# Kernel tuning notes

Hardware: AMD Instinct MI355X
Metric: run time of the kernel (lower is better)

The kernel has to match this reference:

```python
import jax, jax.numpy as jnp
import numpy as np

BRANCH = 4
DEPTH = 8  # complete 4-ary tree, levels 0..8 (leaves are level 0)
X_SIZE = 512
H_SIZE = 512


def _build_tree():
    N = sum(BRANCH ** d for d in range(DEPTH + 1))  # 87381
    depth = np.zeros(N, dtype=np.int32)
    start = 1
    for d in range(1, DEPTH + 1):
        c = BRANCH ** d
        depth[start:start + c] = d
        start += c
    node_level = (DEPTH - depth).astype(np.int32)  # topological height, leaves=0
    src = np.arange(1, N, dtype=np.int32)          # child
    dst = (src - 1) // BRANCH                      # parent
    return N, src, dst.astype(np.int32), node_level


def setup_inputs() -> dict:
    key = jax.random.key(0)
    k = jax.random.split(key, 6)
    N, src, dst, node_level = _build_tree()
    sx = 1.0 / np.sqrt(X_SIZE)
    sh = 1.0 / np.sqrt(H_SIZE)
    return {
        "x": jax.random.normal(k[0], (N, X_SIZE), jnp.float32),
        "W_w": jax.random.normal(k[1], (3 * H_SIZE, X_SIZE), jnp.float32) * sx,
        "b_w": jax.random.normal(k[2], (3 * H_SIZE,), jnp.float32) * sx,
        "U_r": jax.random.normal(k[3], (H_SIZE, H_SIZE), jnp.float32) * sh,
        "U_hc": jax.random.normal(k[4], (H_SIZE, H_SIZE), jnp.float32) * sh,
        "U_z": jax.random.normal(k[5], (H_SIZE, H_SIZE), jnp.float32) * sh,
        "edge_src": jnp.asarray(src),
        "edge_dst": jnp.asarray(dst),
        "node_level": jnp.asarray(node_level),
        "num_levels": DEPTH + 1,
    }


def reference(x, W_w, b_w, U_r, U_hc, U_z, edge_src, edge_dst, node_level, num_levels):
    hs = U_r.shape[0]
    n = x.shape[0]
    wx = x @ W_w.T + b_w                      # (n, 3h)
    wrx = wx[:, :hs]
    whx = wx[:, hs:2 * hs]
    wzx = wx[:, 2 * hs:]
    edge_level = node_level[edge_dst]         # level of parent receiving the message

    # Leaves: mailbox is a single zero 'z' slot -> z = sigmoid(w_z_x), h_pre = 0
    h_leaf = (1.0 - jax.nn.sigmoid(wzx)) * jnp.tanh(whx)
    h = jnp.where((node_level == 0)[:, None], h_leaf, 0.0)

    for l in range(1, num_levels):
        emask = (edge_level == l).astype(x.dtype)[:, None]   # (E,1)
        hsrc = h[edge_src] * emask                            # masked child states (E,h)
        h_sum = jax.ops.segment_sum(hsrc, edge_dst, num_segments=n)  # sum of children
        r = jax.nn.sigmoid(wrx + h_sum @ U_r.T)
        h_cand = jnp.tanh(whx + (r * h_sum) @ U_hc.T)
        z_e = hsrc @ U_z.T                                    # raw U_z(h_child), (E,h)
        # reduce: h_pre = sum_children z_raw * h_child (no sigmoid, faithful to source)
        h_pre = jax.ops.segment_sum(z_e * hsrc, edge_dst, num_segments=n)
        # update: z = sigmoid(z_raw + w_z_x), summed over children
        z_sig_sum = jax.ops.segment_sum(
            jax.nn.sigmoid(z_e + wzx[edge_dst]) * emask, edge_dst, num_segments=n)
        h_new = h_pre + (1.0 - z_sig_sum) * h_cand
        h = jnp.where((node_level == l)[:, None], h_new, h)
    return h
```

## Files before the change

### kernel.cpp

```cpp
#include <hip/hip_runtime.h>


#define NNODES 87381
#define NINT   21845
#define NLEAF  65536

typedef __attribute__((ext_vector_type(8))) __bf16 bf16x8;
typedef __attribute__((ext_vector_type(4))) float f32x4;

__device__ __forceinline__ float sigmoidf_(float x) { return 1.0f / (1.0f + __expf(-x)); }
__device__ __forceinline__ float tanhf_(float x) { return 2.0f / (1.0f + __expf(-2.0f * x)) - 1.0f; }

__device__ __forceinline__ unsigned short bf_rne(float f) {
  unsigned int u = __float_as_uint(f);
  unsigned int r = u + 0x7FFFu + ((u >> 16) & 1u);
  return (unsigned short)(r >> 16);
}
__device__ __forceinline__ void split2(float f, unsigned short& h, unsigned short& l) {
  h = bf_rne(f);
  l = bf_rne(f - __uint_as_float((unsigned int)h << 16));
}
__device__ __forceinline__ float bf2f(unsigned short h) {
  return __uint_as_float((unsigned int)h << 16);
}

__global__ __launch_bounds__(256) void split_k(const float* __restrict__ s,
                                               unsigned short* __restrict__ hi,
                                               unsigned short* __restrict__ lo, int n4) {
  int i = blockIdx.x * 256 + threadIdx.x;
  if (i >= n4) return;
  float4 v = *(const float4*)(s + (size_t)i * 4);
  ushort4 h, l;
  split2(v.x, h.x, l.x); split2(v.y, h.y, l.y);
  split2(v.z, h.z, l.z); split2(v.w, h.w, l.w);
  *(ushort4*)(hi + (size_t)i * 4) = h;
  *(ushort4*)(lo + (size_t)i * 4) = l;
}

template <bool CLAMP>
__device__ __forceinline__ void stage_tile(const unsigned short* __restrict__ g,
                                           int rows_left, unsigned short* l0,
                                           int lane) {
#pragma unroll
  for (int c = 0; c < 8; ++c) {
    const int lr = c * 16 + (lane >> 2);
    const int gr = CLAMP ? (lr < rows_left ? lr : rows_left - 1) : lr;
    const int sg = (lane & 3) ^ ((lr >> 1) & 3);
    __builtin_amdgcn_global_load_lds(
        (const __attribute__((address_space(1))) void*)(g + (size_t)gr * 512 + sg * 8),
        (__attribute__((address_space(3))) void*)(l0 + c * 512), 16, 0, 0);
  }
}

template <int EPI>
__global__ __launch_bounds__(256) void mgemm(const unsigned short* __restrict__ Ah,
                                             const unsigned short* __restrict__ Al,
                                             const unsigned short* __restrict__ Bh,
                                             const unsigned short* __restrict__ Bl,
                                             float* __restrict__ C, int ldc, int M,
                                             const float* __restrict__ wx, int g0,
                                             const float* __restrict__ bias,
                                             const unsigned short* __restrict__ FH,
                                             const unsigned short* __restrict__ FL,
                                             unsigned short* __restrict__ Oh,
                                             unsigned short* __restrict__ Ol) {
  __shared__ unsigned short As_h[2][128][32];
  __shared__ unsigned short As_l[2][128][32];
  __shared__ unsigned short Bs_h[2][128][32];
  __shared__ unsigned short Bs_l[2][128][32];
  const int t = threadIdx.x;
  const int lane = t & 63, wave = t >> 6;
  const int wm = wave & 1, wn = wave >> 1;
  const int m0 = blockIdx.x * 128, n0 = blockIdx.y * 128;

  f32x4 acc[4][4];
#pragma unroll
  for (int i = 0; i < 4; ++i)
#pragma unroll
    for (int j = 0; j < 4; ++j) acc[i][j] = (f32x4){0.f, 0.f, 0.f, 0.f};

  const int fr = lane & 15, fg = lane >> 4;

  auto stage = [&](int buf, int k0) {
    if (wave == 0)      stage_tile<true >(Ah + (size_t)m0 * 512 + k0, M - m0, &As_h[buf][0][0], lane);
    else if (wave == 1) stage_tile<true >(Al + (size_t)m0 * 512 + k0, M - m0, &As_l[buf][0][0], lane);
    else if (wave == 2) stage_tile<false>(Bh + (size_t)n0 * 512 + k0, 0, &Bs_h[buf][0][0], lane);
    else                stage_tile<false>(Bl + (size_t)n0 * 512 + k0, 0, &Bs_l[buf][0][0], lane);
  };

  auto comp = [&](int buf) {
    bf16x8 ah[4], al[4], bh[4], bl[4];
#pragma unroll
    for (int mt = 0; mt < 4; ++mt) {
      const int row = wm * 64 + mt * 16 + fr;
      const int gp = (fg ^ ((row >> 1) & 3)) * 8;
      ah[mt] = *(const bf16x8*)&As_h[buf][row][gp];
      al[mt] = *(const bf16x8*)&As_l[buf][row][gp];
    }
#pragma unroll
    for (int nt = 0; nt < 4; ++nt) {
      const int row = wn * 64 + nt * 16 + fr;
      const int gp = (fg ^ ((row >> 1) & 3)) * 8;
      bh[nt] = *(const bf16x8*)&Bs_h[buf][row][gp];
      bl[nt] = *(const bf16x8*)&Bs_l[buf][row][gp];
    }
#pragma unroll
    for (int mt = 0; mt < 4; ++mt)
#pragma unroll
      for (int nt = 0; nt < 4; ++nt) {
        acc[mt][nt] = __builtin_amdgcn_mfma_f32_16x16x32_bf16(ah[mt], bh[nt], acc[mt][nt], 0, 0, 0);
        acc[mt][nt] = __builtin_amdgcn_mfma_f32_16x16x32_bf16(ah[mt], bl[nt], acc[mt][nt], 0, 0, 0);
        acc[mt][nt] = __builtin_amdgcn_mfma_f32_16x16x32_bf16(al[mt], bh[nt], acc[mt][nt], 0, 0, 0);
      }
  };

  stage(0, 0);
  __syncthreads();
  for (int kk = 0; kk < 16; kk += 2) {
    stage(1, (kk + 1) * 32);
    comp(0);
    __syncthreads();
    if (kk < 14) stage(0, (kk + 2) * 32);
    comp(1);
    __syncthreads();
  }

  const int ecol = lane & 15;
  const int erow = (lane >> 4) * 4;

  if (EPI == 4) {
#pragma unroll
    for (int mt = 0; mt < 4; ++mt) {
#pragma unroll
      for (int nt = 0; nt < 4; ++nt) {
        const int col = n0 + wn * 64 + nt * 16 + ecol;
        const int row0 = m0 + wm * 64 + mt * 16 + erow;
        if (row0 >= M) continue;
        const int p = row0 >> 2;
        const float wz = wx[(size_t)(g0 + p) * 1536 + 1024 + col];
        float hpre = 0.f, zs = 0.f;
#pragma unroll
        for (int r = 0; r < 4; ++r) {
          const float zev = acc[mt][nt][r];
          const float hch = bias[(size_t)(row0 + r) * 512 + col];
          hpre = fmaf(zev, hch, hpre);
          zs += sigmoidf_(zev + wz);
        }
        float* po = C + (size_t)p * 512 + col;
        const float hc = *po;
        const float res = hpre + (1.f - zs) * hc;
        *po = res;
        unsigned short oh, ol;
        split2(res, oh, ol);
        Oh[(size_t)p * 512 + col] = oh;
        Ol[(size_t)p * 512 + col] = ol;
      }
    }
    return;
  }

#pragma unroll
  for (int mt = 0; mt < 4; ++mt) {
#pragma unroll
    for (int nt = 0; nt < 4; ++nt) {
      const int col = n0 + wn * 64 + nt * 16 + ecol;
#pragma unroll
      for (int r = 0; r < 4; ++r) {
        const int row = m0 + wm * 64 + mt * 16 + erow + r;
        if (row >= M) continue;
        const float v = acc[mt][nt][r];
        if (EPI == 1) {
          const size_t ix = (size_t)row * 512 + col;
          const float hs = bf2f(FH[ix]) + bf2f(FL[ix]);
          const float rg = sigmoidf_(wx[(size_t)(g0 + row) * 1536 + col] + v);
          unsigned short oh, ol;
          split2(rg * hs, oh, ol);
          Oh[ix] = oh;
          Ol[ix] = ol;
        } else if (EPI == 2) {
          C[(size_t)row * ldc + col] = tanhf_(wx[(size_t)(g0 + row) * 1536 + 512 + col] + v);
        } else {
          C[(size_t)row * ldc + col] = v + bias[col];
        }
      }
    }
  }
}

__global__ __launch_bounds__(256) void mleaf(const unsigned short* __restrict__ xh,
                                             const unsigned short* __restrict__ xl,
                                             const unsigned short* __restrict__ Wh,
                                             const unsigned short* __restrict__ Wl,
                                             const float* __restrict__ bw,
                                             float* __restrict__ out,
                                             unsigned short* __restrict__ hcH,
                                             unsigned short* __restrict__ hcL) {
  __shared__ unsigned short As_h[2][128][32];
  __shared__ unsigned short As_l[2][128][32];
  __shared__ unsigned short Bs_h[2][128][32];
  __shared__ unsigned short Bs_l[2][128][32];
  const int t = threadIdx.x;
  const int lane = t & 63, wave = t >> 6;
  const int wm = wave & 1, wn = wave >> 1;
  const int m0 = blockIdx.x * 128, n0 = blockIdx.y * 64;

  f32x4 acch[4][2], accz[4][2];
#pragma unroll
  for (int i = 0; i < 4; ++i)
#pragma unroll
    for (int j = 0; j < 2; ++j) {
      acch[i][j] = (f32x4){0.f, 0.f, 0.f, 0.f};
      accz[i][j] = (f32x4){0.f, 0.f, 0.f, 0.f};
    }

  const int fr = lane & 15, fg = lane >> 4;

  auto stage = [&](int buf, int k0) {
    if (wave == 0) {
      stage_tile<false>(xh + (size_t)m0 * 512 + k0, 0, &As_h[buf][0][0], lane);
    } else if (wave == 1) {
      stage_tile<false>(xl + (size_t)m0 * 512 + k0, 0, &As_l[buf][0][0], lane);
    } else {
      const unsigned short* Ws = (wave == 2) ? Wh : Wl;
      unsigned short* dst = (wave == 2) ? &Bs_h[buf][0][0] : &Bs_l[buf][0][0];
#pragma unroll
      for (int c = 0; c < 8; ++c) {
        const int lr = c * 16 + (lane >> 2);
        const int grow = (lr < 64) ? (512 + n0 + lr) : (1024 + n0 + (lr - 64));
        const int sg = (lane & 3) ^ ((lr >> 1) & 3);
        __builtin_amdgcn_global_load_lds(
            (const __attribute__((address_space(1))) void*)(Ws + (size_t)grow * 512 + k0 + sg * 8),
            (__attribute__((address_space(3))) void*)(dst + c * 512), 16, 0, 0);
      }
    }
  };

  auto comp = [&](int buf) {
    bf16x8 ah[4], al[4], bhh[2], bhl[2], bzh[2], bzl[2];
#pragma unroll
    for (int mt = 0; mt < 4; ++mt) {
      const int row = wm * 64 + mt * 16 + fr;
      const int gp = (fg ^ ((row >> 1) & 3)) * 8;
      ah[mt] = *(const bf16x8*)&As_h[buf][row][gp];
      al[mt] = *(const bf16x8*)&As_l[buf][row][gp];
    }
#pragma unroll
    for (int nt = 0; nt < 2; ++nt) {
      const int rh_ = wn * 32 + nt * 16 + fr;
      const int rz_ = 64 + rh_;
      const int gph = (fg ^ ((rh_ >> 1) & 3)) * 8;
      const int gpz = (fg ^ ((rz_ >> 1) & 3)) * 8;
      bhh[nt] = *(const bf16x8*)&Bs_h[buf][rh_][gph];
      bhl[nt] = *(const bf16x8*)&Bs_l[buf][rh_][gph];
      bzh[nt] = *(const bf16x8*)&Bs_h[buf][rz_][gpz];
      bzl[nt] = *(const bf16x8*)&Bs_l[buf][rz_][gpz];
    }
#pragma unroll
    for (int mt = 0; mt < 4; ++mt)
#pragma unroll
      for (int nt = 0; nt < 2; ++nt) {
        acch[mt][nt] = __builtin_amdgcn_mfma_f32_16x16x32_bf16(ah[mt], bhh[nt], acch[mt][nt], 0, 0, 0);
        acch[mt][nt] = __builtin_amdgcn_mfma_f32_16x16x32_bf16(ah[mt], bhl[nt], acch[mt][nt], 0, 0, 0);
        acch[mt][nt] = __builtin_amdgcn_mfma_f32_16x16x32_bf16(al[mt], bhh[nt], acch[mt][nt], 0, 0, 0);
        accz[mt][nt] = __builtin_amdgcn_mfma_f32_16x16x32_bf16(ah[mt], bzh[nt], accz[mt][nt], 0, 0, 0);
        accz[mt][nt] = __builtin_amdgcn_mfma_f32_16x16x32_bf16(ah[mt], bzl[nt], accz[mt][nt], 0, 0, 0);
        accz[mt][nt] = __builtin_amdgcn_mfma_f32_16x16x32_bf16(al[mt], bzh[nt], accz[mt][nt], 0, 0, 0);
      }
  };

  stage(0, 0);
  __syncthreads();
  for (int kk = 0; kk < 16; kk += 2) {
    stage(1, (kk + 1) * 32);
    comp(0);
    __syncthreads();
    if (kk < 14) stage(0, (kk + 2) * 32);
    comp(1);
    __syncthreads();
  }

  const int ecol = lane & 15;
  const int erow = (lane >> 4) * 4;
#pragma unroll
  for (int mt = 0; mt < 4; ++mt) {
#pragma unroll
    for (int nt = 0; nt < 2; ++nt) {
      const int col = n0 + wn * 32 + nt * 16 + ecol;
      const float bh_ = bw[512 + col];
      const float bz_ = bw[1024 + col];
#pragma unroll
      for (int r = 0; r < 4; ++r) {
        const int row = m0 + wm * 64 + mt * 16 + erow + r;
        const float vh = acch[mt][nt][r] + bh_;
        const float vz = accz[mt][nt][r] + bz_;
        const float hval = (1.f - sigmoidf_(vz)) * tanhf_(vh);
        out[(size_t)(NINT + row) * 512 + col] = hval;
        unsigned short oh, ol;
        split2(hval, oh, ol);
        const size_t ix = (size_t)row * 512 + col;
        hcH[ix] = oh;
        hcL[ix] = ol;
      }
    }
  }
}

__global__ __launch_bounds__(256) void child_sum_k(const float* __restrict__ out,
                                                   int cbase, int nl,
                                                   unsigned short* __restrict__ hH,
                                                   unsigned short* __restrict__ hL) {
  const int idx = blockIdx.x * 256 + threadIdx.x;
  if (idx >= nl * 128) return;
  const int i = idx >> 7;
  const int jq = (idx & 127) << 2;
  const float* b = out + (size_t)(cbase + 4 * i) * 512 + jq;
  const float4 a = *(const float4*)(b);
  const float4 c = *(const float4*)(b + 512);
  const float4 d = *(const float4*)(b + 1024);
  const float4 e = *(const float4*)(b + 1536);
  float4 s;
  s.x = a.x + c.x + d.x + e.x;
  s.y = a.y + c.y + d.y + e.y;
  s.z = a.z + c.z + d.z + e.z;
  s.w = a.w + c.w + d.w + e.w;
  ushort4 sh, sl;
  split2(s.x, sh.x, sl.x); split2(s.y, sh.y, sl.y);
  split2(s.z, sh.z, sl.z); split2(s.w, sh.w, sl.w);
  *(ushort4*)(hH + (size_t)i * 512 + jq) = sh;
  *(ushort4*)(hL + (size_t)i * 512 + jq) = sl;
}

extern "C" void kernel_launch(void* const* d_in, const int* in_sizes, int n_in,
                              void* d_out, int out_size, void* d_ws, size_t ws_size,
                              hipStream_t stream) {
  const float* x   = (const float*)d_in[0];
  const float* Ww  = (const float*)d_in[1];
  const float* bw  = (const float*)d_in[2];
  const float* Ur  = (const float*)d_in[3];
  const float* Uhc = (const float*)d_in[4];
  const float* Uz  = (const float*)d_in[5];
  float* out = (float*)d_out;

  char* p = (char*)d_ws;
  unsigned short* x_hi = (unsigned short*)p;
  unsigned short* x_lo = x_hi + (size_t)NNODES * 512;
  unsigned short* rhH = (unsigned short*)p;
  unsigned short* rhL = rhH + (size_t)16384 * 512;
  p += (size_t)NNODES * 512 * 4;
  float* wx_int = (float*)p;                 p += (size_t)NINT * 1536 * 4;
  unsigned short* hsH = (unsigned short*)p;  p += (size_t)16384 * 512 * 2;
  unsigned short* hsL = (unsigned short*)p;  p += (size_t)16384 * 512 * 2;
  unsigned short* hcH = (unsigned short*)p;  p += (size_t)65536 * 512 * 2;
  unsigned short* hcL = (unsigned short*)p;  p += (size_t)65536 * 512 * 2;
  unsigned short* hc2H = (unsigned short*)p; p += (size_t)16384 * 512 * 2;
  unsigned short* hc2L = (unsigned short*)p; p += (size_t)16384 * 512 * 2;
  unsigned short* W_hi = (unsigned short*)p;   p += (size_t)1536 * 512 * 2;
  unsigned short* W_lo = (unsigned short*)p;   p += (size_t)1536 * 512 * 2;
  unsigned short* Ur_hi = (unsigned short*)p;  p += (size_t)512 * 512 * 2;
  unsigned short* Ur_lo = (unsigned short*)p;  p += (size_t)512 * 512 * 2;
  unsigned short* Uhc_hi = (unsigned short*)p; p += (size_t)512 * 512 * 2;
  unsigned short* Uhc_lo = (unsigned short*)p; p += (size_t)512 * 512 * 2;
  unsigned short* Uz_hi = (unsigned short*)p;  p += (size_t)512 * 512 * 2;
  unsigned short* Uz_lo = (unsigned short*)p;  p += (size_t)512 * 512 * 2;

  split_k<<<(1536 * 512 / 4 + 255) / 256, 256, 0, stream>>>(Ww, W_hi, W_lo, 1536 * 512 / 4);
  split_k<<<(512 * 512 / 4 + 255) / 256, 256, 0, stream>>>(Ur, Ur_hi, Ur_lo, 512 * 512 / 4);
  split_k<<<(512 * 512 / 4 + 255) / 256, 256, 0, stream>>>(Uhc, Uhc_hi, Uhc_lo, 512 * 512 / 4);
  split_k<<<(512 * 512 / 4 + 255) / 256, 256, 0, stream>>>(Uz, Uz_hi, Uz_lo, 512 * 512 / 4);
  split_k<<<((int)((size_t)NNODES * 512 / 4) + 255) / 256, 256, 0, stream>>>(
      x, x_hi, x_lo, (int)((size_t)NNODES * 512 / 4));

  mgemm<3><<<dim3((NINT + 127) / 128, 12), 256, 0, stream>>>(
      x_hi, x_lo, W_hi, W_lo, wx_int, 1536, NINT, nullptr, 0, bw,
      nullptr, nullptr, nullptr, nullptr);

  mleaf<<<dim3(NLEAF / 128, 8), 256, 0, stream>>>(
      x_hi + (size_t)NINT * 512, x_lo + (size_t)NINT * 512, W_hi, W_lo, bw, out, hcH, hcL);

  static const int S[10] = {0, 1, 5, 21, 85, 341, 1365, 5461, 21845, 87381};
  unsigned short *rdH = hcH, *rdL = hcL, *wrH = hc2H, *wrL = hc2L;
  for (int l = 1; l <= 8; ++l) {
    const int d = 8 - l;
    const int pbase = S[d];
    const int nl = S[d + 1] - S[d];
    const int cbase = S[d + 1];
    const int el = 4 * nl;

    child_sum_k<<<(nl * 128 + 255) / 256, 256, 0, stream>>>(out, cbase, nl, hsH, hsL);

    dim3 gr((nl + 127) / 128, 4);
    mgemm<1><<<gr, 256, 0, stream>>>(hsH, hsL, Ur_hi, Ur_lo, nullptr, 512, nl,
                                     wx_int, pbase, nullptr, hsH, hsL, rhH, rhL);
    mgemm<2><<<gr, 256, 0, stream>>>(rhH, rhL, Uhc_hi, Uhc_lo,
                                     out + (size_t)pbase * 512, 512, nl,
                                     wx_int, pbase, nullptr, nullptr, nullptr,
                                     nullptr, nullptr);
    dim3 gz((el + 127) / 128, 4);
    mgemm<4><<<gz, 256, 0, stream>>>(rdH, rdL, Uz_hi, Uz_lo,
                                     out + (size_t)pbase * 512, 512, el,
                                     wx_int, pbase, out + (size_t)cbase * 512,
                                     nullptr, nullptr, wrH, wrL);
    unsigned short* tH = rdH; rdH = wrH; wrH = tH;
    unsigned short* tL = rdL; rdL = wrL; wrL = tL;
  }
}
```

Baseline: 1.759 ms.

## Load weight B-fragments directly from global memory instead of staging through LDS

Both GEMM kernels stop staging the weight (B) tiles in shared memory. Each wave now reads its bf16 hi/lo weight fragments straight from global memory (expected to hit in L2) inside the compute step. All four waves now split the A-tile staging between them. This halves LDS footprint and the staging work, which may raise occupancy. The cost is synchronous global loads inside the MFMA loop, which are not prefetched ahead, and redundant reads of the same weights across waves.

```diff
diff --git a/kernel.cpp b/kernel.cpp
--- a/kernel.cpp
+++ b/kernel.cpp
@@ -38,11 +38,11 @@
 }
 
 template <bool CLAMP>
-__device__ __forceinline__ void stage_tile(const unsigned short* __restrict__ g,
+__device__ __forceinline__ void stage_half(const unsigned short* __restrict__ g,
                                            int rows_left, unsigned short* l0,
-                                           int lane) {
-#pragma unroll
-  for (int c = 0; c < 8; ++c) {
+                                           int lane, int c0) {
+#pragma unroll
+  for (int c = c0; c < c0 + 4; ++c) {
     const int lr = c * 16 + (lane >> 2);
     const int gr = CLAMP ? (lr < rows_left ? lr : rows_left - 1) : lr;
     const int sg = (lane & 3) ^ ((lr >> 1) & 3);
@@ -66,8 +66,6 @@
                                              unsigned short* __restrict__ Ol) {
   __shared__ unsigned short As_h[2][128][32];
   __shared__ unsigned short As_l[2][128][32];
-  __shared__ unsigned short Bs_h[2][128][32];
-  __shared__ unsigned short Bs_l[2][128][32];
   const int t = threadIdx.x;
   const int lane = t & 63, wave = t >> 6;
   const int wm = wave & 1, wn = wave >> 1;
@@ -81,15 +79,25 @@
 
   const int fr = lane & 15, fg = lane >> 4;
 
+  int boff[4];
+#pragma unroll
+  for (int nt = 0; nt < 4; ++nt)
+    boff[nt] = (n0 + wn * 64 + nt * 16 + fr) * 512 + fg * 8;
+
   auto stage = [&](int buf, int k0) {
-    if (wave == 0)      stage_tile<true >(Ah + (size_t)m0 * 512 + k0, M - m0, &As_h[buf][0][0], lane);
-    else if (wave == 1) stage_tile<true >(Al + (size_t)m0 * 512 + k0, M - m0, &As_l[buf][0][0], lane);
-    else if (wave == 2) stage_tile<false>(Bh + (size_t)n0 * 512 + k0, 0, &Bs_h[buf][0][0], lane);
-    else                stage_tile<false>(Bl + (size_t)n0 * 512 + k0, 0, &Bs_l[buf][0][0], lane);
+    if (wave == 0)      stage_half<true>(Ah + (size_t)m0 * 512 + k0, M - m0, &As_h[buf][0][0], lane, 0);
+    else if (wave == 1) stage_half<true>(Ah + (size_t)m0 * 512 + k0, M - m0, &As_h[buf][0][0], lane, 4);
+    else if (wave == 2) stage_half<true>(Al + (size_t)m0 * 512 + k0, M - m0, &As_l[buf][0][0], lane, 0);
+    else                stage_half<true>(Al + (size_t)m0 * 512 + k0, M - m0, &As_l[buf][0][0], lane, 4);
   };
 
-  auto comp = [&](int buf) {
+  auto comp = [&](int buf, int k0) {
     bf16x8 ah[4], al[4], bh[4], bl[4];
+#pragma unroll
+    for (int nt = 0; nt < 4; ++nt) {
+      bh[nt] = *(const bf16x8*)(Bh + (size_t)(boff[nt] + k0));
+      bl[nt] = *(const bf16x8*)(Bl + (size_t)(boff[nt] + k0));
+    }
 #pragma unroll
     for (int mt = 0; mt < 4; ++mt) {
       const int row = wm * 64 + mt * 16 + fr;
@@ -98,13 +106,6 @@
       al[mt] = *(const bf16x8*)&As_l[buf][row][gp];
     }
 #pragma unroll
-    for (int nt = 0; nt < 4; ++nt) {
-      const int row = wn * 64 + nt * 16 + fr;
-      const int gp = (fg ^ ((row >> 1) & 3)) * 8;
-      bh[nt] = *(const bf16x8*)&Bs_h[buf][row][gp];
-      bl[nt] = *(const bf16x8*)&Bs_l[buf][row][gp];
-    }
-#pragma unroll
     for (int mt = 0; mt < 4; ++mt)
 #pragma unroll
       for (int nt = 0; nt < 4; ++nt) {
@@ -118,10 +119,10 @@
   __syncthreads();
   for (int kk = 0; kk < 16; kk += 2) {
     stage(1, (kk + 1) * 32);
-    comp(0);
+    comp(0, kk * 32);
     __syncthreads();
     if (kk < 14) stage(0, (kk + 2) * 32);
-    comp(1);
+    comp(1, (kk + 1) * 32);
     __syncthreads();
   }
 
@@ -197,8 +198,6 @@
                                              unsigned short* __restrict__ hcL) {
   __shared__ unsigned short As_h[2][128][32];
   __shared__ unsigned short As_l[2][128][32];
-  __shared__ unsigned short Bs_h[2][128][32];
-  __shared__ unsigned short Bs_l[2][128][32];
   const int t = threadIdx.x;
   const int lane = t & 63, wave = t >> 6;
   const int wm = wave & 1, wn = wave >> 1;
@@ -215,45 +214,35 @@
 
   const int fr = lane & 15, fg = lane >> 4;
 
+  int boffh[2], boffz[2];
+#pragma unroll
+  for (int nt = 0; nt < 2; ++nt) {
+    boffh[nt] = (512 + n0 + wn * 32 + nt * 16 + fr) * 512 + fg * 8;
+    boffz[nt] = (1024 + n0 + wn * 32 + nt * 16 + fr) * 512 + fg * 8;
+  }
+
   auto stage = [&](int buf, int k0) {
-    if (wave == 0) {
-      stage_tile<false>(xh + (size_t)m0 * 512 + k0, 0, &As_h[buf][0][0], lane);
-    } else if (wave == 1) {
-      stage_tile<false>(xl + (size_t)m0 * 512 + k0, 0, &As_l[buf][0][0], lane);
-    } else {
-      const unsigned short* Ws = (wave == 2) ? Wh : Wl;
-      unsigned short* dst = (wave == 2) ? &Bs_h[buf][0][0] : &Bs_l[buf][0][0];
-#pragma unroll
-      for (int c = 0; c < 8; ++c) {
-        const int lr = c * 16 + (lane >> 2);
-        const int grow = (lr < 64) ? (512 + n0 + lr) : (1024 + n0 + (lr - 64));
-        const int sg = (lane & 3) ^ ((lr >> 1) & 3);
-        __builtin_amdgcn_global_load_lds(
-            (const __attribute__((address_space(1))) void*)(Ws + (size_t)grow * 512 + k0 + sg * 8),
-            (__attribute__((address_space(3))) void*)(dst + c * 512), 16, 0, 0);
-      }
-    }
+    if (wave == 0)      stage_half<false>(xh + (size_t)m0 * 512 + k0, 0, &As_h[buf][0][0], lane, 0);
+    else if (wave == 1) stage_half<false>(xh + (size_t)m0 * 512 + k0, 0, &As_h[buf][0][0], lane, 4);
+    else if (wave == 2) stage_half<false>(xl + (size_t)m0 * 512 + k0, 0, &As_l[buf][0][0], lane, 0);
+    else                stage_half<false>(xl + (size_t)m0 * 512 + k0, 0, &As_l[buf][0][0], lane, 4);
   };
 
-  auto comp = [&](int buf) {
+  auto comp = [&](int buf, int k0) {
     bf16x8 ah[4], al[4], bhh[2], bhl[2], bzh[2], bzl[2];
+#pragma unroll
+    for (int nt = 0; nt < 2; ++nt) {
+      bhh[nt] = *(const bf16x8*)(Wh + (size_t)(boffh[nt] + k0));
+      bhl[nt] = *(const bf16x8*)(Wl + (size_t)(boffh[nt] + k0));
+      bzh[nt] = *(const bf16x8*)(Wh + (size_t)(boffz[nt] + k0));
+      bzl[nt] = *(const bf16x8*)(Wl + (size_t)(boffz[nt] + k0));
+    }
 #pragma unroll
     for (int mt = 0; mt < 4; ++mt) {
       const int row = wm * 64 + mt * 16 + fr;
       const int gp = (fg ^ ((row >> 1) & 3)) * 8;
       ah[mt] = *(const bf16x8*)&As_h[buf][row][gp];
       al[mt] = *(const bf16x8*)&As_l[buf][row][gp];
-    }
-#pragma unroll
-    for (int nt = 0; nt < 2; ++nt) {
-      const int rh_ = wn * 32 + nt * 16 + fr;
-      const int rz_ = 64 + rh_;
-      const int gph = (fg ^ ((rh_ >> 1) & 3)) * 8;
-      const int gpz = (fg ^ ((rz_ >> 1) & 3)) * 8;
-      bhh[nt] = *(const bf16x8*)&Bs_h[buf][rh_][gph];
-      bhl[nt] = *(const bf16x8*)&Bs_l[buf][rh_][gph];
-      bzh[nt] = *(const bf16x8*)&Bs_h[buf][rz_][gpz];
-      bzl[nt] = *(const bf16x8*)&Bs_l[buf][rz_][gpz];
     }
 #pragma unroll
     for (int mt = 0; mt < 4; ++mt)
@@ -272,10 +261,10 @@
   __syncthreads();
   for (int kk = 0; kk < 16; kk += 2) {
     stage(1, (kk + 1) * 32);
-    comp(0);
+    comp(0, kk * 32);
     __syncthreads();
     if (kk < 14) stage(0, (kk + 2) * 32);
-    comp(1);
+    comp(1, (kk + 1) * 32);
     __syncthreads();
   }
 
```

Measured after the change: 2.226 ms. 26.6% more time.

## Use 8 waves per block in MFMA GEMM kernels with halved per-wave tiles

Applied to the files above, without the earlier changes.

Doubles block size from 256 to 512 threads in mgemm and mleaf, splitting each 128x128 (or 128x64 pair) output tile across 8 waves so each wave holds half the accumulators. Staging is split so two waves load each of the four hi/lo A/B tiles. The aim is more waves per CU to hide LDS and global latency and lower register pressure per wave. The cost is less operand reuse per wave, meaning more LDS reads per MFMA, and the launch_bounds(512,4) constraint may force spills.

```diff
diff --git a/kernel.cpp b/kernel.cpp
--- a/kernel.cpp
+++ b/kernel.cpp
@@ -38,11 +38,11 @@
 }
 
 template <bool CLAMP>
-__device__ __forceinline__ void stage_tile(const unsigned short* __restrict__ g,
+__device__ __forceinline__ void stage_half(const unsigned short* __restrict__ g,
                                            int rows_left, unsigned short* l0,
-                                           int lane) {
-#pragma unroll
-  for (int c = 0; c < 8; ++c) {
+                                           int lane, int c0) {
+#pragma unroll
+  for (int c = c0; c < c0 + 4; ++c) {
     const int lr = c * 16 + (lane >> 2);
     const int gr = CLAMP ? (lr < rows_left ? lr : rows_left - 1) : lr;
     const int sg = (lane & 3) ^ ((lr >> 1) & 3);
@@ -53,17 +53,17 @@
 }
 
 template <int EPI>
-__global__ __launch_bounds__(256) void mgemm(const unsigned short* __restrict__ Ah,
-                                             const unsigned short* __restrict__ Al,
-                                             const unsigned short* __restrict__ Bh,
-                                             const unsigned short* __restrict__ Bl,
-                                             float* __restrict__ C, int ldc, int M,
-                                             const float* __restrict__ wx, int g0,
-                                             const float* __restrict__ bias,
-                                             const unsigned short* __restrict__ FH,
-                                             const unsigned short* __restrict__ FL,
-                                             unsigned short* __restrict__ Oh,
-                                             unsigned short* __restrict__ Ol) {
+__global__ __launch_bounds__(512, 4) void mgemm(const unsigned short* __restrict__ Ah,
+                                                const unsigned short* __restrict__ Al,
+                                                const unsigned short* __restrict__ Bh,
+                                                const unsigned short* __restrict__ Bl,
+                                                float* __restrict__ C, int ldc, int M,
+                                                const float* __restrict__ wx, int g0,
+                                                const float* __restrict__ bias,
+                                                const unsigned short* __restrict__ FH,
+                                                const unsigned short* __restrict__ FL,
+                                                unsigned short* __restrict__ Oh,
+                                                unsigned short* __restrict__ Ol) {
   __shared__ unsigned short As_h[2][128][32];
   __shared__ unsigned short As_l[2][128][32];
   __shared__ unsigned short Bs_h[2][128][32];
@@ -73,23 +73,26 @@
   const int wm = wave & 1, wn = wave >> 1;
   const int m0 = blockIdx.x * 128, n0 = blockIdx.y * 128;
 
-  f32x4 acc[4][4];
+  f32x4 acc[4][2];
 #pragma unroll
   for (int i = 0; i < 4; ++i)
 #pragma unroll
-    for (int j = 0; j < 4; ++j) acc[i][j] = (f32x4){0.f, 0.f, 0.f, 0.f};
+    for (int j = 0; j < 2; ++j) acc[i][j] = (f32x4){0.f, 0.f, 0.f, 0.f};
 
   const int fr = lane & 15, fg = lane >> 4;
 
   auto stage = [&](int buf, int k0) {
-    if (wave == 0)      stage_tile<true >(Ah + (size_t)m0 * 512 + k0, M - m0, &As_h[buf][0][0], lane);
-    else if (wave == 1) stage_tile<true >(Al + (size_t)m0 * 512 + k0, M - m0, &As_l[buf][0][0], lane);
-    else if (wave == 2) stage_tile<false>(Bh + (size_t)n0 * 512 + k0, 0, &Bs_h[buf][0][0], lane);
-    else                stage_tile<false>(Bl + (size_t)n0 * 512 + k0, 0, &Bs_l[buf][0][0], lane);
+    const int c0 = (wave & 1) * 4;
+    switch (wave >> 1) {
+      case 0: stage_half<true >(Ah + (size_t)m0 * 512 + k0, M - m0, &As_h[buf][0][0], lane, c0); break;
+      case 1: stage_half<true >(Al + (size_t)m0 * 512 + k0, M - m0, &As_l[buf][0][0], lane, c0); break;
+      case 2: stage_half<false>(Bh + (size_t)n0 * 512 + k0, 0, &Bs_h[buf][0][0], lane, c0); break;
+      default: stage_half<false>(Bl + (size_t)n0 * 512 + k0, 0, &Bs_l[buf][0][0], lane, c0); break;
+    }
   };
 
   auto comp = [&](int buf) {
-    bf16x8 ah[4], al[4], bh[4], bl[4];
+    bf16x8 ah[4], al[4], bh[2], bl[2];
 #pragma unroll
     for (int mt = 0; mt < 4; ++mt) {
       const int row = wm * 64 + mt * 16 + fr;
@@ -98,8 +101,8 @@
       al[mt] = *(const bf16x8*)&As_l[buf][row][gp];
     }
 #pragma unroll
-    for (int nt = 0; nt < 4; ++nt) {
-      const int row = wn * 64 + nt * 16 + fr;
+    for (int nt = 0; nt < 2; ++nt) {
+      const int row = wn * 32 + nt * 16 + fr;
       const int gp = (fg ^ ((row >> 1) & 3)) * 8;
       bh[nt] = *(const bf16x8*)&Bs_h[buf][row][gp];
       bl[nt] = *(const bf16x8*)&Bs_l[buf][row][gp];
@@ -107,7 +110,7 @@
 #pragma unroll
     for (int mt = 0; mt < 4; ++mt)
 #pragma unroll
-      for (int nt = 0; nt < 4; ++nt) {
+      for (int nt = 0; nt < 2; ++nt) {
         acc[mt][nt] = __builtin_amdgcn_mfma_f32_16x16x32_bf16(ah[mt], bh[nt], acc[mt][nt], 0, 0, 0);
         acc[mt][nt] = __builtin_amdgcn_mfma_f32_16x16x32_bf16(ah[mt], bl[nt], acc[mt][nt], 0, 0, 0);
         acc[mt][nt] = __builtin_amdgcn_mfma_f32_16x16x32_bf16(al[mt], bh[nt], acc[mt][nt], 0, 0, 0);
@@ -132,8 +135,8 @@
 #pragma unroll
     for (int mt = 0; mt < 4; ++mt) {
 #pragma unroll
-      for (int nt = 0; nt < 4; ++nt) {
-        const int col = n0 + wn * 64 + nt * 16 + ecol;
+      for (int nt = 0; nt < 2; ++nt) {
+        const int col = n0 + wn * 32 + nt * 16 + ecol;
         const int row0 = m0 + wm * 64 + mt * 16 + erow;
         if (row0 >= M) continue;
         const int p = row0 >> 2;
@@ -162,8 +165,8 @@
 #pragma unroll
   for (int mt = 0; mt < 4; ++mt) {
 #pragma unroll
-    for (int nt = 0; nt < 4; ++nt) {
-      const int col = n0 + wn * 64 + nt * 16 + ecol;
+    for (int nt = 0; nt < 2; ++nt) {
+      const int col = n0 + wn * 32 + nt * 16 + ecol;
 #pragma unroll
       for (int r = 0; r < 4; ++r) {
         const int row = m0 + wm * 64 + mt * 16 + erow + r;
@@ -187,14 +190,14 @@
   }
 }
 
-__global__ __launch_bounds__(256) void mleaf(const unsigned short* __restrict__ xh,
-                                             const unsigned short* __restrict__ xl,
-                                             const unsigned short* __restrict__ Wh,
-                                             const unsigned short* __restrict__ Wl,
-                                             const float* __restrict__ bw,
-                                             float* __restrict__ out,
-                                             unsigned short* __restrict__ hcH,
-                                             unsigned short* __restrict__ hcL) {
+__global__ __launch_bounds__(512, 4) void mleaf(const unsigned short* __restrict__ xh,
+                                                const unsigned short* __restrict__ xl,
+                                                const unsigned short* __restrict__ Wh,
+                                                const unsigned short* __restrict__ Wl,
+                                                const float* __restrict__ bw,
+                                                float* __restrict__ out,
+                                                unsigned short* __restrict__ hcH,
+                                                unsigned short* __restrict__ hcL) {
   __shared__ unsigned short As_h[2][128][32];
   __shared__ unsigned short As_l[2][128][32];
   __shared__ unsigned short Bs_h[2][128][32];
@@ -204,27 +207,27 @@
   const int wm = wave & 1, wn = wave >> 1;
   const int m0 = blockIdx.x * 128, n0 = blockIdx.y * 64;
 
-  f32x4 acch[4][2], accz[4][2];
-#pragma unroll
-  for (int i = 0; i < 4; ++i)
-#pragma unroll
-    for (int j = 0; j < 2; ++j) {
-      acch[i][j] = (f32x4){0.f, 0.f, 0.f, 0.f};
-      accz[i][j] = (f32x4){0.f, 0.f, 0.f, 0.f};
-    }
+  f32x4 acch[4], accz[4];
+#pragma unroll
+  for (int i = 0; i < 4; ++i) {
+    acch[i] = (f32x4){0.f, 0.f, 0.f, 0.f};
+    accz[i] = (f32x4){0.f, 0.f, 0.f, 0.f};
+  }
 
   const int fr = lane & 15, fg = lane >> 4;
 
   auto stage = [&](int buf, int k0) {
-    if (wave == 0) {
-      stage_tile<false>(xh + (size_t)m0 * 512 + k0, 0, &As_h[buf][0][0], lane);
-    } else if (wave == 1) {
-      stage_tile<false>(xl + (size_t)m0 * 512 + k0, 0, &As_l[buf][0][0], lane);
+    const int c0 = (wave & 1) * 4;
+    const int grp = wave >> 1;
+    if (grp == 0) {
+      stage_half<false>(xh + (size_t)m0 * 512 + k0, 0, &As_h[buf][0][0], lane, c0);
+    } else if (grp == 1) {
+      stage_half<false>(xl + (size_t)m0 * 512 + k0, 0, &As_l[buf][0][0], lane, c0);
     } else {
-      const unsigned short* Ws = (wave == 2) ? Wh : Wl;
-      unsigned short* dst = (wave == 2) ? &Bs_h[buf][0][0] : &Bs_l[buf][0][0];
-#pragma unroll
-      for (int c = 0; c < 8; ++c) {
+      const unsigned short* Ws = (grp == 2) ? Wh : Wl;
+      unsigned short* dst = (grp == 2) ? &Bs_h[buf][0][0] : &Bs_l[buf][0][0];
+#pragma unroll
+      for (int c = c0; c < c0 + 4; ++c) {
         const int lr = c * 16 + (lane >> 2);
         const int grow = (lr < 64) ? (512 + n0 + lr) : (1024 + n0 + (lr - 64));
         const int sg = (lane & 3) ^ ((lr >> 1) & 3);
@@ -236,7 +239,17 @@
   };
 
   auto comp = [&](int buf) {
-    bf16x8 ah[4], al[4], bhh[2], bhl[2], bzh[2], bzl[2];
+    bf16x8 ah[4], al[4], bhh, bhl, bzh, bzl;
+    {
+      const int rh_ = wn * 16 + fr;
+      const int rz_ = 64 + rh_;
+      const int gph = (fg ^ ((rh_ >> 1) & 3)) * 8;
+      const int gpz = (fg ^ ((rz_ >> 1) & 3)) * 8;
+      bhh = *(const bf16x8*)&Bs_h[buf][rh_][gph];
+      bhl = *(const bf16x8*)&Bs_l[buf][rh_][gph];
+      bzh = *(const bf16x8*)&Bs_h[buf][rz_][gpz];
+      bzl = *(const bf16x8*)&Bs_l[buf][rz_][gpz];
+    }
 #pragma unroll
     for (int mt = 0; mt < 4; ++mt) {
       const int row = wm * 64 + mt * 16 + fr;
@@ -245,27 +258,14 @@
       al[mt] = *(const bf16x8*)&As_l[buf][row][gp];
     }
 #pragma unroll
-    for (int nt = 0; nt < 2; ++nt) {
-      const int rh_ = wn * 32 + nt * 16 + fr;
-      const int rz_ = 64 + rh_;
-      const int gph = (fg ^ ((rh_ >> 1) & 3)) * 8;
-      const int gpz = (fg ^ ((rz_ >> 1) & 3)) * 8;
-      bhh[nt] = *(const bf16x8*)&Bs_h[buf][rh_][gph];
-      bhl[nt] = *(const bf16x8*)&Bs_l[buf][rh_][gph];
-      bzh[nt] = *(const bf16x8*)&Bs_h[buf][rz_][gpz];
-      bzl[nt] = *(const bf16x8*)&Bs_l[buf][rz_][gpz];
-    }
-#pragma unroll
-    for (int mt = 0; mt < 4; ++mt)
-#pragma unroll
-      for (int nt = 0; nt < 2; ++nt) {
-        acch[mt][nt] = __builtin_amdgcn_mfma_f32_16x16x32_bf16(ah[mt], bhh[nt], acch[mt][nt], 0, 0, 0);
-        acch[mt][nt] = __builtin_amdgcn_mfma_f32_16x16x32_bf16(ah[mt], bhl[nt], acch[mt][nt], 0, 0, 0);
-        acch[mt][nt] = __builtin_amdgcn_mfma_f32_16x16x32_bf16(al[mt], bhh[nt], acch[mt][nt], 0, 0, 0);
-        accz[mt][nt] = __builtin_amdgcn_mfma_f32_16x16x32_bf16(ah[mt], bzh[nt], accz[mt][nt], 0, 0, 0);
-        accz[mt][nt] = __builtin_amdgcn_mfma_f32_16x16x32_bf16(ah[mt], bzl[nt], accz[mt][nt], 0, 0, 0);
-        accz[mt][nt] = __builtin_amdgcn_mfma_f32_16x16x32_bf16(al[mt], bzh[nt], accz[mt][nt], 0, 0, 0);
-      }
+    for (int mt = 0; mt < 4; ++mt) {
+      acch[mt] = __builtin_amdgcn_mfma_f32_16x16x32_bf16(ah[mt], bhh, acch[mt], 0, 0, 0);
+      acch[mt] = __builtin_amdgcn_mfma_f32_16x16x32_bf16(ah[mt], bhl, acch[mt], 0, 0, 0);
+      acch[mt] = __builtin_amdgcn_mfma_f32_16x16x32_bf16(al[mt], bhh, acch[mt], 0, 0, 0);
+      accz[mt] = __builtin_amdgcn_mfma_f32_16x16x32_bf16(ah[mt], bzh, accz[mt], 0, 0, 0);
+      accz[mt] = __builtin_amdgcn_mfma_f32_16x16x32_bf16(ah[mt], bzl, accz[mt], 0, 0, 0);
+      accz[mt] = __builtin_amdgcn_mfma_f32_16x16x32_bf16(al[mt], bzh, accz[mt], 0, 0, 0);
+    }
   };
 
   stage(0, 0);
@@ -281,26 +281,23 @@
 
   const int ecol = lane & 15;
   const int erow = (lane >> 4) * 4;
+  const int col = n0 + wn * 16 + ecol;
+  const float bh_ = bw[512 + col];
+  const float bz_ = bw[1024 + col];
 #pragma unroll
   for (int mt = 0; mt < 4; ++mt) {
 #pragma unroll
-    for (int nt = 0; nt < 2; ++nt) {
-      const int col = n0 + wn * 32 + nt * 16 + ecol;
-      const float bh_ = bw[512 + col];
-      const float bz_ = bw[1024 + col];
-#pragma unroll
-      for (int r = 0; r < 4; ++r) {
-        const int row = m0 + wm * 64 + mt * 16 + erow + r;
-        const float vh = acch[mt][nt][r] + bh_;
-        const float vz = accz[mt][nt][r] + bz_;
-        const float hval = (1.f - sigmoidf_(vz)) * tanhf_(vh);
-        out[(size_t)(NINT + row) * 512 + col] = hval;
-        unsigned short oh, ol;
-        split2(hval, oh, ol);
-        const size_t ix = (size_t)row * 512 + col;
-        hcH[ix] = oh;
-        hcL[ix] = ol;
-      }
+    for (int r = 0; r < 4; ++r) {
+      const int row = m0 + wm * 64 + mt * 16 + erow + r;
+      const float vh = acch[mt][r] + bh_;
+      const float vz = accz[mt][r] + bz_;
+      const float hval = (1.f - sigmoidf_(vz)) * tanhf_(vh);
+      out[(size_t)(NINT + row) * 512 + col] = hval;
+      unsigned short oh, ol;
+      split2(hval, oh, ol);
+      const size_t ix = (size_t)row * 512 + col;
+      hcH[ix] = oh;
+      hcL[ix] = ol;
     }
   }
 }
@@ -370,11 +367,11 @@
   split_k<<<((int)((size_t)NNODES * 512 / 4) + 255) / 256, 256, 0, stream>>>(
       x, x_hi, x_lo, (int)((size_t)NNODES * 512 / 4));
 
-  mgemm<3><<<dim3((NINT + 127) / 128, 12), 256, 0, stream>>>(
+  mgemm<3><<<dim3((NINT + 127) / 128, 12), 512, 0, stream>>>(
       x_hi, x_lo, W_hi, W_lo, wx_int, 1536, NINT, nullptr, 0, bw,
       nullptr, nullptr, nullptr, nullptr);
 
-  mleaf<<<dim3(NLEAF / 128, 8), 256, 0, stream>>>(
+  mleaf<<<dim3(NLEAF / 128, 8), 512, 0, stream>>>(
       x_hi + (size_t)NINT * 512, x_lo + (size_t)NINT * 512, W_hi, W_lo, bw, out, hcH, hcL);
 
   static const int S[10] = {0, 1, 5, 21, 85, 341, 1365, 5461, 21845, 87381};
@@ -389,14 +386,14 @@
     child_sum_k<<<(nl * 128 + 255) / 256, 256, 0, stream>>>(out, cbase, nl, hsH, hsL);
 
     dim3 gr((nl + 127) / 128, 4);
-    mgemm<1><<<gr, 256, 0, stream>>>(hsH, hsL, Ur_hi, Ur_lo, nullptr, 512, nl,
+    mgemm<1><<<gr, 512, 0, stream>>>(hsH, hsL, Ur_hi, Ur_lo, nullptr, 512, nl,
                                      wx_int, pbase, nullptr, hsH, hsL, rhH, rhL);
-    mgemm<2><<<gr, 256, 0, stream>>>(rhH, rhL, Uhc_hi, Uhc_lo,
+    mgemm<2><<<gr, 512, 0, stream>>>(rhH, rhL, Uhc_hi, Uhc_lo,
                                      out + (size_t)pbase * 512, 512, nl,
                                      wx_int, pbase, nullptr, nullptr, nullptr,
                                      nullptr, nullptr);
     dim3 gz((el + 127) / 128, 4);
-    mgemm<4><<<gz, 256, 0, stream>>>(rdH, rdL, Uz_hi, Uz_lo,
+    mgemm<4><<<gz, 512, 0, stream>>>(rdH, rdL, Uz_hi, Uz_lo,
                                      out + (size_t)pbase * 512, 512, el,
                                      wx_int, pbase, out + (size_t)cbase * 512,
                                      nullptr, nullptr, wrH, wrL);
```

Result: faster. 1.459 ms (-17.0%).
